# Kernel optimization log

Hardware: AMD Instinct MI355X
Metric: run time of the kernel (lower is better)

The kernel has to match this reference:

```python
import jax, jax.numpy as jnp
import numpy as np

B = 65536          # batch (number of states)
M = 32             # obstacles per state -> x width = 2*M
PHI = [4, 64, 64, 64]
RHO = [64, 64, 64, 32]


def _init_mlp(key, dims, prefix):
    params = {}
    ks = jax.random.split(key, len(dims) - 1)
    for i, (din, dout) in enumerate(zip(dims[:-1], dims[1:])):
        scale = 1.0 / np.sqrt(din)
        params[f"{prefix}_W{i+1}"] = scale * jax.random.normal(ks[i], (din, dout), dtype=jnp.float32)
        params[f"{prefix}_b{i+1}"] = jnp.zeros((dout,), dtype=jnp.float32)
    return params


def setup_inputs() -> dict:
    key = jax.random.key(0)
    kx, kv, kphi, krho = jax.random.split(key, 4)
    inp = {
        "x": jax.random.normal(kx, (B, 2 * M), dtype=jnp.float32),
        "vel": jax.random.normal(kv, (B, 2), dtype=jnp.float32),
    }
    inp.update(_init_mlp(kphi, PHI, "phi"))
    inp.update(_init_mlp(krho, RHO, "rho"))
    return inp


def _mlp3(h, W1, b1, W2, b2, W3, b3):
    # FeedForward: activation between hidden layers, linear output
    h = jax.nn.relu(h @ W1 + b1)
    h = jax.nn.relu(h @ W2 + b2)
    return h @ W3 + b3


def reference(x, vel,
              phi_W1, phi_b1, phi_W2, phi_b2, phi_W3, phi_b3,
              rho_W1, rho_b1, rho_W2, rho_b2, rho_W3, rho_b3):
    b = x.shape[0]
    m = x.shape[1] // 2
    obs = x.reshape(b, m, 2)                                   # [B, M, 2]
    velb = jnp.broadcast_to(vel[:, None, :], (b, m, 2))        # [B, M, 2]
    inp = jnp.concatenate([obs, velb], axis=-1)                # [B, M, 4]
    # phi batched across all obstacle elements (replaces the per-i loop)
    h = _mlp3(inp, phi_W1, phi_b1, phi_W2, phi_b2, phi_W3, phi_b3)  # [B, M, 64]
    X = h.sum(axis=1)                                          # DeepSets sum pool -> [B, 64]
    return _mlp3(X, rho_W1, rho_b1, rho_W2, rho_b2, rho_W3, rho_b3)  # [B, 32]
```

## Files before the change

### kernel.cpp

```cpp
#include <hip/hip_runtime.h>

typedef _Float16 h16x8 __attribute__((ext_vector_type(8)));
typedef _Float16 h16x4 __attribute__((ext_vector_type(4)));
typedef _Float16 h16x2 __attribute__((ext_vector_type(2)));
typedef float    fx4   __attribute__((ext_vector_type(4)));

static __device__ __forceinline__ fx4 mfma16(h16x8 a, h16x8 b, fx4 c) {
  return __builtin_amdgcn_mfma_f32_16x16x32_f16(a, b, c, 0, 0, 0);
}
static __device__ __forceinline__ h16x2 pkrtz(float a, float b) {
  auto r = __builtin_amdgcn_cvt_pkrtz(a, b);
  h16x2 o; __builtin_memcpy(&o, &r, sizeof(o)); return o;
}
static __device__ __forceinline__ h16x2 splat2(float v) {
  const _Float16 h = (_Float16)v; h16x2 r; r[0] = h; r[1] = h; return r;
}
union ABfrag { h16x2 p[4]; h16x8 v; };
union H4     { h16x2 p[2]; h16x4 v; };


__global__ __launch_bounds__(64, 2)
void deepset_main(const float* __restrict__ x,   const float* __restrict__ vel,
                  const float* __restrict__ pW1, const float* __restrict__ pb1,
                  const float* __restrict__ pW2, const float* __restrict__ pb2,
                  const float* __restrict__ pW3, const float* __restrict__ pb3,
                  const float* __restrict__ rW1, const float* __restrict__ rb1,
                  const float* __restrict__ rW2, const float* __restrict__ rb2,
                  const float* __restrict__ rW3, const float* __restrict__ rb3,
                  float* __restrict__ out)
{
  __shared__ __align__(16) float    xT[16][68];
  __shared__ __align__(16) _Float16 h2T[16][72];

  const int lane = threadIdx.x & 63;
  const int q    = lane >> 4;
  const int c    = lane & 15;
  const int sBase = blockIdx.x * 16;

  {
    const int s0 = lane >> 2, ch = lane & 3;
#pragma unroll
    for (int k = 0; k < 4; ++k) {
      const float4 g = ((const float4*)x)[(size_t)(sBase + s0)*16 + ch + 4*k];
      *(float4*)&xT[s0][(ch + 4*k)*4] = g;
    }
  }
  const float2 vc = *(const float2*)(vel + 2*(size_t)(sBase + c));

  h16x2 wx[2][4], wy[2][4], vbp[2][4];
#pragma unroll
  for (int ks = 0; ks < 2; ++ks)
#pragma unroll
    for (int t = 0; t < 4; ++t) {
      const int f0 = 32*ks + 8*q + 2*t;
      wx[ks][t] = pkrtz(pW1[f0], pW1[f0 + 1]);
      wy[ks][t] = pkrtz(pW1[64 + f0], pW1[64 + f0 + 1]);
      const float v0 = fmaf(vc.x, pW1[128 + f0],     fmaf(vc.y, pW1[192 + f0],     pb1[f0]));
      const float v1 = fmaf(vc.x, pW1[128 + f0 + 1], fmaf(vc.y, pW1[192 + f0 + 1], pb1[f0 + 1]));
      vbp[ks][t] = pkrtz(v0, v1);
    }

  h16x8 B2[4][2];
#pragma unroll
  for (int ct = 0; ct < 4; ++ct)
#pragma unroll
    for (int ks = 0; ks < 2; ++ks) {
      ABfrag a;
#pragma unroll
      for (int t = 0; t < 4; ++t) {
        const int p0 = 32*ks + 8*q + 2*t;
        a.p[t] = pkrtz(pW2[p0*64 + 16*ct + c], pW2[(p0 + 1)*64 + 16*ct + c]);
      }
      B2[ct][ks] = a.v;
    }
  float b2v[4];
#pragma unroll
  for (int ct = 0; ct < 4; ++ct) b2v[ct] = pb2[16*ct + c];

  __builtin_amdgcn_s_waitcnt(0xC07F);
  __builtin_amdgcn_wave_barrier();

  const h16x2 z2 = splat2(0.f);
  float Xacc[4][4] = {};

  float4 p_cur = *(const float4*)&xT[c][0];
#pragma unroll 1
  for (int oo = 0; oo < 16; ++oo) {
    float4 p_nxt;
    if (oo < 15) p_nxt = *(const float4*)&xT[c][4*(oo + 1)];
#pragma unroll
    for (int hh = 0; hh < 2; ++hh) {
      const h16x2 ox = splat2(hh ? p_cur.z : p_cur.x);
      const h16x2 oy = splat2(hh ? p_cur.w : p_cur.y);
      h16x8 A1[2];
#pragma unroll
      for (int ks = 0; ks < 2; ++ks) {
        ABfrag a;
#pragma unroll
        for (int t = 0; t < 4; ++t) {
          const h16x2 h = ox * wx[ks][t] + oy * wy[ks][t] + vbp[ks][t];
          a.p[t] = __builtin_elementwise_max(h, z2);
        }
        A1[ks] = a.v;
      }
#pragma unroll
      for (int ct = 0; ct < 4; ++ct) {
        fx4 acc = {b2v[ct], b2v[ct], b2v[ct], b2v[ct]};
        acc = mfma16(A1[0], B2[ct][0], acc);
        acc = mfma16(A1[1], B2[ct][1], acc);
#pragma unroll
        for (int r = 0; r < 4; ++r)
          Xacc[ct][r] += fmaxf(acc[r], 0.f);
      }
    }
    p_cur = p_nxt;
  }

#pragma unroll
  for (int r = 0; r < 4; ++r) {
    H4 pk;
    pk.p[0] = pkrtz(Xacc[0][r], Xacc[1][r]);
    pk.p[1] = pkrtz(Xacc[2][r], Xacc[3][r]);
    *(h16x4*)&h2T[4*q + r][4*c] = pk.v;
  }

  h16x8 B3[4][2];
#pragma unroll
  for (int ct = 0; ct < 4; ++ct)
#pragma unroll
    for (int ks = 0; ks < 2; ++ks) {
      ABfrag a;
#pragma unroll
      for (int t = 0; t < 4; ++t) {
        const int p0 = 32*ks + 8*q + 2*t;
        const int f0 = 16*(p0 & 3) + (p0 >> 2);
        const int f1 = 16*((p0 + 1) & 3) + ((p0 + 1) >> 2);
        a.p[t] = pkrtz(pW3[f0*64 + 16*ct + c], pW3[f1*64 + 16*ct + c]);
      }
      B3[ct][ks] = a.v;
    }
  float b3s[4];
#pragma unroll
  for (int ct = 0; ct < 4; ++ct) b3s[ct] = 32.f * pb3[16*ct + c];

  __builtin_amdgcn_s_waitcnt(0xC07F);
  __builtin_amdgcn_wave_barrier();
  h16x8 AX[2];
#pragma unroll
  for (int ks = 0; ks < 2; ++ks)
    AX[ks] = *(const h16x8*)&h2T[c][32*ks + 8*q];
  __builtin_amdgcn_wave_barrier();

  fx4 C3[4];
#pragma unroll
  for (int ct = 0; ct < 4; ++ct) {
    fx4 acc = {b3s[ct], b3s[ct], b3s[ct], b3s[ct]};
    acc = mfma16(AX[0], B3[ct][0], acc);
    acc = mfma16(AX[1], B3[ct][1], acc);
    C3[ct] = acc;
  }
#pragma unroll
  for (int r = 0; r < 4; ++r) {
    H4 pk;
    pk.p[0] = pkrtz(C3[0][r], C3[1][r]);
    pk.p[1] = pkrtz(C3[2][r], C3[3][r]);
    *(h16x4*)&h2T[4*q + r][4*c] = pk.v;
  }

  h16x8 R1[4][2];
#pragma unroll
  for (int ct = 0; ct < 4; ++ct)
#pragma unroll
    for (int ks = 0; ks < 2; ++ks) {
      ABfrag a;
#pragma unroll
      for (int t = 0; t < 4; ++t) {
        const int p0 = 32*ks + 8*q + 2*t;
        const int f0 = 16*(p0 & 3) + (p0 >> 2);
        const int f1 = 16*((p0 + 1) & 3) + ((p0 + 1) >> 2);
        a.p[t] = pkrtz(rW1[f0*64 + 16*ct + c], rW1[f1*64 + 16*ct + c]);
      }
      R1[ct][ks] = a.v;
    }
  float rb1v[4];
#pragma unroll
  for (int ct = 0; ct < 4; ++ct) rb1v[ct] = rb1[16*ct + c];

  __builtin_amdgcn_s_waitcnt(0xC07F);
  __builtin_amdgcn_wave_barrier();
  h16x8 A1r[2];
#pragma unroll
  for (int ks = 0; ks < 2; ++ks)
    A1r[ks] = *(const h16x8*)&h2T[c][32*ks + 8*q];
  __builtin_amdgcn_wave_barrier();

  fx4 D1[4];
#pragma unroll
  for (int ct = 0; ct < 4; ++ct) {
    fx4 acc = {rb1v[ct], rb1v[ct], rb1v[ct], rb1v[ct]};
    acc = mfma16(A1r[0], R1[ct][0], acc);
    acc = mfma16(A1r[1], R1[ct][1], acc);
    D1[ct] = acc;
  }
#pragma unroll
  for (int r = 0; r < 4; ++r) {
    H4 pk;
    pk.p[0] = pkrtz(fmaxf(D1[0][r], 0.f), fmaxf(D1[1][r], 0.f));
    pk.p[1] = pkrtz(fmaxf(D1[2][r], 0.f), fmaxf(D1[3][r], 0.f));
    *(h16x4*)&h2T[4*q + r][4*c] = pk.v;
  }

  h16x8 R2[4][2];
#pragma unroll
  for (int ct = 0; ct < 4; ++ct)
#pragma unroll
    for (int ks = 0; ks < 2; ++ks) {
      ABfrag a;
#pragma unroll
      for (int t = 0; t < 4; ++t) {
        const int p0 = 32*ks + 8*q + 2*t;
        const int f0 = 16*(p0 & 3) + (p0 >> 2);
        const int f1 = 16*((p0 + 1) & 3) + ((p0 + 1) >> 2);
        a.p[t] = pkrtz(rW2[f0*64 + 16*ct + c], rW2[f1*64 + 16*ct + c]);
      }
      R2[ct][ks] = a.v;
    }
  float rb2v[4];
#pragma unroll
  for (int ct = 0; ct < 4; ++ct) rb2v[ct] = rb2[16*ct + c];

  __builtin_amdgcn_s_waitcnt(0xC07F);
  __builtin_amdgcn_wave_barrier();
  h16x8 A2r[2];
#pragma unroll
  for (int ks = 0; ks < 2; ++ks)
    A2r[ks] = *(const h16x8*)&h2T[c][32*ks + 8*q];
  __builtin_amdgcn_wave_barrier();

  fx4 D2[4];
#pragma unroll
  for (int ct = 0; ct < 4; ++ct) {
    fx4 acc = {rb2v[ct], rb2v[ct], rb2v[ct], rb2v[ct]};
    acc = mfma16(A2r[0], R2[ct][0], acc);
    acc = mfma16(A2r[1], R2[ct][1], acc);
    D2[ct] = acc;
  }
#pragma unroll
  for (int r = 0; r < 4; ++r) {
    H4 pk;
    pk.p[0] = pkrtz(fmaxf(D2[0][r], 0.f), fmaxf(D2[1][r], 0.f));
    pk.p[1] = pkrtz(fmaxf(D2[2][r], 0.f), fmaxf(D2[3][r], 0.f));
    *(h16x4*)&h2T[4*q + r][4*c] = pk.v;
  }

  h16x8 R3[2][2];
#pragma unroll
  for (int ct = 0; ct < 2; ++ct)
#pragma unroll
    for (int ks = 0; ks < 2; ++ks) {
      ABfrag a;
#pragma unroll
      for (int t = 0; t < 4; ++t) {
        const int p0 = 32*ks + 8*q + 2*t;
        const int f0 = 16*(p0 & 3) + (p0 >> 2);
        const int f1 = 16*((p0 + 1) & 3) + ((p0 + 1) >> 2);
        a.p[t] = pkrtz(rW3[f0*32 + 16*ct + c], rW3[f1*32 + 16*ct + c]);
      }
      R3[ct][ks] = a.v;
    }
  float rb3v[2];
#pragma unroll
  for (int ct = 0; ct < 2; ++ct) rb3v[ct] = rb3[16*ct + c];

  __builtin_amdgcn_s_waitcnt(0xC07F);
  __builtin_amdgcn_wave_barrier();
  h16x8 A3r[2];
#pragma unroll
  for (int ks = 0; ks < 2; ++ks)
    A3r[ks] = *(const h16x8*)&h2T[c][32*ks + 8*q];
  __builtin_amdgcn_wave_barrier();

  fx4 D3[2];
#pragma unroll
  for (int ct = 0; ct < 2; ++ct) {
    fx4 acc = {rb3v[ct], rb3v[ct], rb3v[ct], rb3v[ct]};
    acc = mfma16(A3r[0], R3[ct][0], acc);
    acc = mfma16(A3r[1], R3[ct][1], acc);
    D3[ct] = acc;
  }
  const int srow = sBase + 4*q;
#pragma unroll
  for (int ct = 0; ct < 2; ++ct)
#pragma unroll
    for (int r = 0; r < 4; ++r)
      out[(size_t)(srow + r)*32 + 16*ct + c] = D3[ct][r];
}

extern "C" void kernel_launch(void* const* d_in, const int* in_sizes, int n_in,
                              void* d_out, int out_size, void* d_ws, size_t ws_size,
                              hipStream_t stream) {
  const float* x   = (const float*)d_in[0];
  const float* vel = (const float*)d_in[1];
  const float* pW1 = (const float*)d_in[2];
  const float* pb1 = (const float*)d_in[3];
  const float* pW2 = (const float*)d_in[4];
  const float* pb2 = (const float*)d_in[5];
  const float* pW3 = (const float*)d_in[6];
  const float* pb3 = (const float*)d_in[7];
  const float* rW1 = (const float*)d_in[8];
  const float* rb1 = (const float*)d_in[9];
  const float* rW2 = (const float*)d_in[10];
  const float* rb2 = (const float*)d_in[11];
  const float* rW3 = (const float*)d_in[12];
  const float* rb3 = (const float*)d_in[13];
  float* out = (float*)d_out;

  const int B = in_sizes[0] / 64;
  deepset_main<<<dim3(B / 16), dim3(64), 0, stream>>>(
      x, vel, pW1, pb1, pW2, pb2, pW3, pb3,
      rW1, rb1, rW2, rb2, rW3, rb3, out);
}
```

Baseline: 127.0 us.

## Use 8-wave blocks sharing fp16 weight tiles staged once in LDS

The block grows from one wave handling 16 states to eight waves handling 128 states. The phi/rho weight matrices (W2, W3, rho W1-W3) are loaded once per block with vector loads, converted to fp16 and transposed into shared memory. Each wave then reads its MFMA B fragments from shared memory instead of issuing many scalar strided global loads with per-element conversion. The x tile is converted to fp16 before it goes into shared memory, and the ReLU/accumulate steps use vector max. This adds a block-wide __syncthreads, uses more LDS per block and changes the occupancy trade-off.

```diff
diff --git a/kernel.cpp b/kernel.cpp
--- a/kernel.cpp
+++ b/kernel.cpp
@@ -12,14 +12,11 @@
   auto r = __builtin_amdgcn_cvt_pkrtz(a, b);
   h16x2 o; __builtin_memcpy(&o, &r, sizeof(o)); return o;
 }
-static __device__ __forceinline__ h16x2 splat2(float v) {
-  const _Float16 h = (_Float16)v; h16x2 r; r[0] = h; r[1] = h; return r;
-}
 union ABfrag { h16x2 p[4]; h16x8 v; };
 union H4     { h16x2 p[2]; h16x4 v; };
 
 
-__global__ __launch_bounds__(64, 2)
+__global__ __launch_bounds__(512, 4)
 void deepset_main(const float* __restrict__ x,   const float* __restrict__ vel,
                   const float* __restrict__ pW1, const float* __restrict__ pb1,
                   const float* __restrict__ pW2, const float* __restrict__ pb2,
@@ -29,23 +26,68 @@
                   const float* __restrict__ rW3, const float* __restrict__ rb3,
                   float* __restrict__ out)
 {
-  __shared__ __align__(16) float    xT[16][68];
-  __shared__ __align__(16) _Float16 h2T[16][72];
-
-  const int lane = threadIdx.x & 63;
+  __shared__ __align__(16) _Float16 L2T[64][72];
+  __shared__ __align__(16) _Float16 L3T[64][72];
+  __shared__ __align__(16) _Float16 Q1T[64][72];
+  __shared__ __align__(16) _Float16 Q2T[64][72];
+  __shared__ __align__(16) _Float16 Q3T[32][72];
+  __shared__ __align__(16) _Float16 xh[8][16][72];
+
+  const int tid  = threadIdx.x;
+  const int wave = tid >> 6;
+  const int lane = tid & 63;
   const int q    = lane >> 4;
   const int c    = lane & 15;
-  const int sBase = blockIdx.x * 16;
+  const int sBase = blockIdx.x * 128;
+  const int sWave = sBase + wave * 16;
 
   {
-    const int s0 = lane >> 2, ch = lane & 3;
+    const int p  = tid >> 3;
+    const int cg = (tid & 7) * 8;
+    const int f  = 16*(p & 3) + (p >> 2);
+    const fx4 w2a = *(const fx4*)(pW2 + p*64 + cg);
+    const fx4 w2b = *(const fx4*)(pW2 + p*64 + cg + 4);
+    const fx4 w3a = *(const fx4*)(pW3 + f*64 + cg);
+    const fx4 w3b = *(const fx4*)(pW3 + f*64 + cg + 4);
+    const fx4 r1a = *(const fx4*)(rW1 + f*64 + cg);
+    const fx4 r1b = *(const fx4*)(rW1 + f*64 + cg + 4);
+    const fx4 r2a = *(const fx4*)(rW2 + f*64 + cg);
+    const fx4 r2b = *(const fx4*)(rW2 + f*64 + cg + 4);
+#pragma unroll
+    for (int i = 0; i < 4; ++i) {
+      L2T[cg + i][p]     = (_Float16)w2a[i];
+      L2T[cg + 4 + i][p] = (_Float16)w2b[i];
+      L3T[cg + i][p]     = (_Float16)w3a[i];
+      L3T[cg + 4 + i][p] = (_Float16)w3b[i];
+      Q1T[cg + i][p]     = (_Float16)r1a[i];
+      Q1T[cg + 4 + i][p] = (_Float16)r1b[i];
+      Q2T[cg + i][p]     = (_Float16)r2a[i];
+      Q2T[cg + 4 + i][p] = (_Float16)r2b[i];
+    }
+    if (tid < 256) {
+      const int p3  = tid >> 2;
+      const int cg3 = (tid & 3) * 8;
+      const int f3  = 16*(p3 & 3) + (p3 >> 2);
+      const fx4 r3a = *(const fx4*)(rW3 + f3*32 + cg3);
+      const fx4 r3b = *(const fx4*)(rW3 + f3*32 + cg3 + 4);
+#pragma unroll
+      for (int i = 0; i < 4; ++i) {
+        Q3T[cg3 + i][p3]     = (_Float16)r3a[i];
+        Q3T[cg3 + 4 + i][p3] = (_Float16)r3b[i];
+      }
+    }
+  }
+
+  {
+    const int s0 = lane >> 2, ch = (lane & 3) * 16;
 #pragma unroll
     for (int k = 0; k < 4; ++k) {
-      const float4 g = ((const float4*)x)[(size_t)(sBase + s0)*16 + ch + 4*k];
-      *(float4*)&xT[s0][(ch + 4*k)*4] = g;
-    }
-  }
-  const float2 vc = *(const float2*)(vel + 2*(size_t)(sBase + c));
+      const fx4 g = *(const fx4*)(x + (size_t)(sWave + s0)*64 + ch + 4*k);
+      H4 pk; pk.p[0] = pkrtz(g[0], g[1]); pk.p[1] = pkrtz(g[2], g[3]);
+      *(h16x4*)&xh[wave][s0][ch + 4*k] = pk.v;
+    }
+  }
+  const float2 vc = *(const float2*)(vel + 2*(size_t)(sWave + c));
 
   h16x2 wx[2][4], wy[2][4], vbp[2][4];
 #pragma unroll
@@ -59,39 +101,33 @@
       const float v1 = fmaf(vc.x, pW1[128 + f0 + 1], fmaf(vc.y, pW1[192 + f0 + 1], pb1[f0 + 1]));
       vbp[ks][t] = pkrtz(v0, v1);
     }
+  float b2v[4];
+#pragma unroll
+  for (int ct = 0; ct < 4; ++ct) b2v[ct] = pb2[16*ct + c];
+
+  __syncthreads();
 
   h16x8 B2[4][2];
 #pragma unroll
   for (int ct = 0; ct < 4; ++ct)
 #pragma unroll
-    for (int ks = 0; ks < 2; ++ks) {
-      ABfrag a;
-#pragma unroll
-      for (int t = 0; t < 4; ++t) {
-        const int p0 = 32*ks + 8*q + 2*t;
-        a.p[t] = pkrtz(pW2[p0*64 + 16*ct + c], pW2[(p0 + 1)*64 + 16*ct + c]);
-      }
-      B2[ct][ks] = a.v;
-    }
-  float b2v[4];
-#pragma unroll
-  for (int ct = 0; ct < 4; ++ct) b2v[ct] = pb2[16*ct + c];
-
-  __builtin_amdgcn_s_waitcnt(0xC07F);
-  __builtin_amdgcn_wave_barrier();
-
-  const h16x2 z2 = splat2(0.f);
-  float Xacc[4][4] = {};
-
-  float4 p_cur = *(const float4*)&xT[c][0];
+    for (int ks = 0; ks < 2; ++ks)
+      B2[ct][ks] = *(const h16x8*)&L2T[16*ct + c][32*ks + 8*q];
+
+  const h16x2 z2 = {(_Float16)0.f, (_Float16)0.f};
+  const fx4 zf4 = {0.f, 0.f, 0.f, 0.f};
+  fx4 Xacc[4] = {zf4, zf4, zf4, zf4};
+
+  h16x4 p_cur = *(const h16x4*)&xh[wave][c][0];
 #pragma unroll 1
   for (int oo = 0; oo < 16; ++oo) {
-    float4 p_nxt;
-    if (oo < 15) p_nxt = *(const float4*)&xT[c][4*(oo + 1)];
+    h16x4 p_nxt;
+    if (oo < 15) p_nxt = *(const h16x4*)&xh[wave][c][4*(oo + 1)];
 #pragma unroll
     for (int hh = 0; hh < 2; ++hh) {
-      const h16x2 ox = splat2(hh ? p_cur.z : p_cur.x);
-      const h16x2 oy = splat2(hh ? p_cur.w : p_cur.y);
+      h16x2 ox, oy;
+      ox[0] = p_cur[2*hh];     ox[1] = p_cur[2*hh];
+      oy[0] = p_cur[2*hh + 1]; oy[1] = p_cur[2*hh + 1];
       h16x8 A1[2];
 #pragma unroll
       for (int ks = 0; ks < 2; ++ks) {
@@ -108,13 +144,13 @@
         fx4 acc = {b2v[ct], b2v[ct], b2v[ct], b2v[ct]};
         acc = mfma16(A1[0], B2[ct][0], acc);
         acc = mfma16(A1[1], B2[ct][1], acc);
-#pragma unroll
-        for (int r = 0; r < 4; ++r)
-          Xacc[ct][r] += fmaxf(acc[r], 0.f);
+        Xacc[ct] += __builtin_elementwise_max(acc, zf4);
       }
     }
     p_cur = p_nxt;
   }
+
+  _Float16 (*h2T)[72] = xh[wave];
 
 #pragma unroll
   for (int r = 0; r < 4; ++r) {
@@ -123,22 +159,12 @@
     pk.p[1] = pkrtz(Xacc[2][r], Xacc[3][r]);
     *(h16x4*)&h2T[4*q + r][4*c] = pk.v;
   }
-
   h16x8 B3[4][2];
 #pragma unroll
   for (int ct = 0; ct < 4; ++ct)
 #pragma unroll
-    for (int ks = 0; ks < 2; ++ks) {
-      ABfrag a;
-#pragma unroll
-      for (int t = 0; t < 4; ++t) {
-        const int p0 = 32*ks + 8*q + 2*t;
-        const int f0 = 16*(p0 & 3) + (p0 >> 2);
-        const int f1 = 16*((p0 + 1) & 3) + ((p0 + 1) >> 2);
-        a.p[t] = pkrtz(pW3[f0*64 + 16*ct + c], pW3[f1*64 + 16*ct + c]);
-      }
-      B3[ct][ks] = a.v;
-    }
+    for (int ks = 0; ks < 2; ++ks)
+      B3[ct][ks] = *(const h16x8*)&L3T[16*ct + c][32*ks + 8*q];
   float b3s[4];
 #pragma unroll
   for (int ct = 0; ct < 4; ++ct) b3s[ct] = 32.f * pb3[16*ct + c];
@@ -166,22 +192,12 @@
     pk.p[1] = pkrtz(C3[2][r], C3[3][r]);
     *(h16x4*)&h2T[4*q + r][4*c] = pk.v;
   }
-
   h16x8 R1[4][2];
 #pragma unroll
   for (int ct = 0; ct < 4; ++ct)
 #pragma unroll
-    for (int ks = 0; ks < 2; ++ks) {
-      ABfrag a;
-#pragma unroll
-      for (int t = 0; t < 4; ++t) {
-        const int p0 = 32*ks + 8*q + 2*t;
-        const int f0 = 16*(p0 & 3) + (p0 >> 2);
-        const int f1 = 16*((p0 + 1) & 3) + ((p0 + 1) >> 2);
-        a.p[t] = pkrtz(rW1[f0*64 + 16*ct + c], rW1[f1*64 + 16*ct + c]);
-      }
-      R1[ct][ks] = a.v;
-    }
+    for (int ks = 0; ks < 2; ++ks)
+      R1[ct][ks] = *(const h16x8*)&Q1T[16*ct + c][32*ks + 8*q];
   float rb1v[4];
 #pragma unroll
   for (int ct = 0; ct < 4; ++ct) rb1v[ct] = rb1[16*ct + c];
@@ -200,31 +216,21 @@
     fx4 acc = {rb1v[ct], rb1v[ct], rb1v[ct], rb1v[ct]};
     acc = mfma16(A1r[0], R1[ct][0], acc);
     acc = mfma16(A1r[1], R1[ct][1], acc);
-    D1[ct] = acc;
+    D1[ct] = __builtin_elementwise_max(acc, zf4);
   }
 #pragma unroll
   for (int r = 0; r < 4; ++r) {
     H4 pk;
-    pk.p[0] = pkrtz(fmaxf(D1[0][r], 0.f), fmaxf(D1[1][r], 0.f));
-    pk.p[1] = pkrtz(fmaxf(D1[2][r], 0.f), fmaxf(D1[3][r], 0.f));
+    pk.p[0] = pkrtz(D1[0][r], D1[1][r]);
+    pk.p[1] = pkrtz(D1[2][r], D1[3][r]);
     *(h16x4*)&h2T[4*q + r][4*c] = pk.v;
   }
-
   h16x8 R2[4][2];
 #pragma unroll
   for (int ct = 0; ct < 4; ++ct)
 #pragma unroll
-    for (int ks = 0; ks < 2; ++ks) {
-      ABfrag a;
-#pragma unroll
-      for (int t = 0; t < 4; ++t) {
-        const int p0 = 32*ks + 8*q + 2*t;
-        const int f0 = 16*(p0 & 3) + (p0 >> 2);
-        const int f1 = 16*((p0 + 1) & 3) + ((p0 + 1) >> 2);
-        a.p[t] = pkrtz(rW2[f0*64 + 16*ct + c], rW2[f1*64 + 16*ct + c]);
-      }
-      R2[ct][ks] = a.v;
-    }
+    for (int ks = 0; ks < 2; ++ks)
+      R2[ct][ks] = *(const h16x8*)&Q2T[16*ct + c][32*ks + 8*q];
   float rb2v[4];
 #pragma unroll
   for (int ct = 0; ct < 4; ++ct) rb2v[ct] = rb2[16*ct + c];
@@ -243,31 +249,21 @@
     fx4 acc = {rb2v[ct], rb2v[ct], rb2v[ct], rb2v[ct]};
     acc = mfma16(A2r[0], R2[ct][0], acc);
     acc = mfma16(A2r[1], R2[ct][1], acc);
-    D2[ct] = acc;
+    D2[ct] = __builtin_elementwise_max(acc, zf4);
   }
 #pragma unroll
   for (int r = 0; r < 4; ++r) {
     H4 pk;
-    pk.p[0] = pkrtz(fmaxf(D2[0][r], 0.f), fmaxf(D2[1][r], 0.f));
-    pk.p[1] = pkrtz(fmaxf(D2[2][r], 0.f), fmaxf(D2[3][r], 0.f));
+    pk.p[0] = pkrtz(D2[0][r], D2[1][r]);
+    pk.p[1] = pkrtz(D2[2][r], D2[3][r]);
     *(h16x4*)&h2T[4*q + r][4*c] = pk.v;
   }
-
   h16x8 R3[2][2];
 #pragma unroll
   for (int ct = 0; ct < 2; ++ct)
 #pragma unroll
-    for (int ks = 0; ks < 2; ++ks) {
-      ABfrag a;
-#pragma unroll
-      for (int t = 0; t < 4; ++t) {
-        const int p0 = 32*ks + 8*q + 2*t;
-        const int f0 = 16*(p0 & 3) + (p0 >> 2);
-        const int f1 = 16*((p0 + 1) & 3) + ((p0 + 1) >> 2);
-        a.p[t] = pkrtz(rW3[f0*32 + 16*ct + c], rW3[f1*32 + 16*ct + c]);
-      }
-      R3[ct][ks] = a.v;
-    }
+    for (int ks = 0; ks < 2; ++ks)
+      R3[ct][ks] = *(const h16x8*)&Q3T[16*ct + c][32*ks + 8*q];
   float rb3v[2];
 #pragma unroll
   for (int ct = 0; ct < 2; ++ct) rb3v[ct] = rb3[16*ct + c];
@@ -288,7 +284,7 @@
     acc = mfma16(A3r[1], R3[ct][1], acc);
     D3[ct] = acc;
   }
-  const int srow = sBase + 4*q;
+  const int srow = sWave + 4*q;
 #pragma unroll
   for (int ct = 0; ct < 2; ++ct)
 #pragma unroll
@@ -316,7 +312,7 @@
   float* out = (float*)d_out;
 
   const int B = in_sizes[0] / 64;
-  deepset_main<<<dim3(B / 16), dim3(64), 0, stream>>>(
+  deepset_main<<<dim3(B / 128), dim3(512), 0, stream>>>(
       x, vel, pW1, pb1, pW2, pb2, pW3, pb3,
       rW1, rb1, rW2, rb2, rW3, rb3, out);
 }
```

After: 121.7 us. -4.2%, faster.
